# Optimization experiments

Hardware: AMD Instinct MI355X
Metric: run time of the kernel (lower is better)

## Reference

```python
import jax, jax.numpy as jnp
from jax import lax
import numpy as np

VOCAB = 100000
EMB = 256
HID = 512          # bidirectional total
H = HID // 2       # per-direction hidden
TAGS = 12
START_IDX = 10
STOP_IDX = 11
B, S = 32, 256
NEG = -10000.0


def setup_inputs() -> dict:
    key = jax.random.key(0)
    ks = jax.random.split(key, 14)
    sc = 0.1
    sentences = jax.random.randint(ks[0], (B, S), 0, VOCAB)
    emb = jax.random.normal(ks[1], (VOCAB, EMB), jnp.float32) * sc
    wih_f = jax.random.normal(ks[2], (4 * H, EMB), jnp.float32) * sc
    whh_f = jax.random.normal(ks[3], (4 * H, H), jnp.float32) * sc
    bih_f = jax.random.normal(ks[4], (4 * H,), jnp.float32) * sc
    bhh_f = jax.random.normal(ks[5], (4 * H,), jnp.float32) * sc
    wih_b = jax.random.normal(ks[6], (4 * H, EMB), jnp.float32) * sc
    whh_b = jax.random.normal(ks[7], (4 * H, H), jnp.float32) * sc
    bih_b = jax.random.normal(ks[8], (4 * H,), jnp.float32) * sc
    bhh_b = jax.random.normal(ks[9], (4 * H,), jnp.float32) * sc
    w_out = jax.random.normal(ks[10], (TAGS, HID), jnp.float32) * sc
    b_out = jax.random.normal(ks[11], (TAGS,), jnp.float32) * sc
    transitions = jax.random.normal(ks[12], (TAGS, TAGS), jnp.float32)
    transitions = transitions.at[START_IDX, :].set(NEG)   # never transition into START
    transitions = transitions.at[:, STOP_IDX].set(NEG)    # never transition out of STOP
    return dict(sentences=sentences, emb=emb, wih_f=wih_f, whh_f=whh_f,
                bih_f=bih_f, bhh_f=bhh_f, wih_b=wih_b, whh_b=whh_b,
                bih_b=bih_b, bhh_b=bhh_b, w_out=w_out, b_out=b_out,
                transitions=transitions)


def _lstm_dir(x, wih, whh, bih, bhh, reverse):
    # x: [B,S,E]; PyTorch gate order i,f,g,o
    xg = jnp.einsum('bse,ge->bsg', x, wih) + bih + bhh  # [B,S,4H]
    h0 = jnp.zeros((x.shape[0], whh.shape[1]), x.dtype)
    c0 = jnp.zeros_like(h0)

    def step(carry, g_t):
        h, c = carry
        g = g_t + h @ whh.T
        i, f, gg, o = jnp.split(g, 4, axis=-1)
        c = jax.nn.sigmoid(f) * c + jax.nn.sigmoid(i) * jnp.tanh(gg)
        h = jax.nn.sigmoid(o) * jnp.tanh(c)
        return (h, c), h

    _, hs = lax.scan(step, (h0, c0), jnp.swapaxes(xg, 0, 1), reverse=reverse)
    return jnp.swapaxes(hs, 0, 1)  # [B,S,H]


def _features(sentences, emb, wih_f, whh_f, bih_f, bhh_f,
              wih_b, whh_b, bih_b, bhh_b, w_out, b_out):
    x = emb[sentences]                                   # [B,S,E]
    hf = _lstm_dir(x, wih_f, whh_f, bih_f, bhh_f, False)
    hb = _lstm_dir(x, wih_b, whh_b, bih_b, bhh_b, True)
    h = jnp.concatenate([hf, hb], axis=-1)               # [B,S,HID]
    return jnp.einsum('bsh,th->bst', h, w_out) + b_out   # [B,S,TAGS]


def _viterbi(feats, transitions):
    # feats: [B,S,T]; returns (score [B], path [B,S] int32)
    T = feats.shape[-1]
    init = jnp.full((T,), NEG, feats.dtype).at[START_IDX].set(0.0)

    def step(fv, emit):
        scores = fv[None, :] + transitions               # [next_tag, prev_tag]
        bp = jnp.argmax(scores, axis=1).astype(jnp.int32)
        fv_new = jnp.max(scores, axis=1) + emit
        return fv_new, bp

    def per_seq(feat_seq):                               # [S,T]
        fv, bps = lax.scan(step, init, feat_seq)         # bps: [S,T]
        term = fv + transitions[STOP_IDX]
        best = jnp.argmax(term).astype(jnp.int32)
        score = term[best]

        def back(tag, bp_t):
            return bp_t[tag], tag

        _, path = lax.scan(back, best, bps, reverse=True)
        return score, path

    return jax.vmap(per_seq)(feats)


def reference(sentences, emb, wih_f, whh_f, bih_f, bhh_f,
              wih_b, whh_b, bih_b, bhh_b, w_out, b_out, transitions):
    feats = _features(sentences, emb, wih_f, whh_f, bih_f, bhh_f,
                      wih_b, whh_b, bih_b, bhh_b, w_out, b_out)
    score, path = _viterbi(feats, transitions)
    return score, path
```

## Files before the change

kernel.cpp:

```cpp
#include <hip/hip_runtime.h>
#include <math.h>

#define BATCH 32
#define SEQ 256
#define EMBD 256
#define HDIM 256
#define G4H 1024
#define TAGS 12
#define START_IDX 10
#define STOP_IDX 11
#define NEGV -10000.0f

#define KRES 48
#define KLDS_G 18
#define KSTR_G 34

#define WS_XG    0
#define WS_X     16777216
#define WS_WPACK 18874368
#define WS_HALL  19234816
#define WS_FEATS 23429120

__device__ __forceinline__ float bcast(float v, int l) {
    return __int_as_float(__builtin_amdgcn_readlane(__float_as_int(v), l));
}

__global__ void gather_x(const int* __restrict__ sent, const float* __restrict__ emb,
                         float* __restrict__ x) {
    int m = blockIdx.x;
    int lane = threadIdx.x;
    long long row = sent[m];
    float4 v = *(const float4*)(emb + row * EMBD + lane * 4);
    *(float4*)(x + (size_t)m * EMBD + lane * 4) = v;
}

__global__ void pack_whh(const float* __restrict__ whh_f, const float* __restrict__ whh_b,
                         float4* __restrict__ pack) {
    int idx = blockIdx.x * 256 + threadIdx.x;
    if (idx >= 2 * 2 * KSTR_G * 512) return;
    int g = idx & 511;
    int r = idx >> 9;
    int j = r % KSTR_G; r /= KSTR_G;
    int half = r & 1, dir = r >> 1;
    int R = (g >> 7) * 256 + half * 128 + (g & 127);
    const float* w = dir ? whh_b : whh_f;
    pack[idx] = *(const float4*)(w + (size_t)R * HDIM + KRES + 4 * KLDS_G + 4 * j);
}

__launch_bounds__(256)
__global__ void gemm_xg(const float* __restrict__ x,
                        const float* __restrict__ wih_f, const float* __restrict__ wih_b,
                        const float* __restrict__ bih_f, const float* __restrict__ bhh_f,
                        const float* __restrict__ bih_b, const float* __restrict__ bhh_b,
                        float* __restrict__ xg) {
    __shared__ __align__(16) float as[8][128];
    __shared__ __align__(16) float bs[8][128];
    int m0 = blockIdx.x * 128;
    int n0 = blockIdx.y * 128;
    int tid = threadIdx.x;
    int tx = tid & 15, ty = tid >> 4;
    int lr = tid >> 1;
    int lh = (tid & 1) * 4;

    const float* arow = x + (size_t)(m0 + lr) * EMBD;
    const float* brow;
    {
        int n = n0 + lr;
        const float* w = (n < G4H) ? wih_f : wih_b;
        brow = w + (size_t)(n & 1023) * EMBD;
    }

    float acc[8][8];
    #pragma unroll
    for (int i = 0; i < 8; i++)
        #pragma unroll
        for (int j = 0; j < 8; j++) acc[i][j] = 0.f;

    for (int k0 = 0; k0 < EMBD; k0 += 8) {
        float4 av = *(const float4*)(arow + k0 + lh);
        float4 bv = *(const float4*)(brow + k0 + lh);
        __syncthreads();
        as[lh + 0][lr] = av.x; as[lh + 1][lr] = av.y; as[lh + 2][lr] = av.z; as[lh + 3][lr] = av.w;
        bs[lh + 0][lr] = bv.x; bs[lh + 1][lr] = bv.y; bs[lh + 2][lr] = bv.z; bs[lh + 3][lr] = bv.w;
        __syncthreads();
        #pragma unroll
        for (int kk = 0; kk < 8; kk++) {
            float4 a0 = *(const float4*)&as[kk][ty * 8];
            float4 a1 = *(const float4*)&as[kk][ty * 8 + 4];
            float4 b0 = *(const float4*)&bs[kk][tx * 8];
            float4 b1 = *(const float4*)&bs[kk][tx * 8 + 4];
            float a[8] = {a0.x, a0.y, a0.z, a0.w, a1.x, a1.y, a1.z, a1.w};
            float b[8] = {b0.x, b0.y, b0.z, b0.w, b1.x, b1.y, b1.z, b1.w};
            #pragma unroll
            for (int i = 0; i < 8; i++)
                #pragma unroll
                for (int j = 0; j < 8; j++) acc[i][j] += a[i] * b[j];
        }
    }

    int n = n0 + tx * 8;
    int dir = n >> 10, g0 = n & 1023;
    const float* bih = dir ? bih_b : bih_f;
    const float* bhh = dir ? bhh_b : bhh_f;
    float bi[8], bh[8];
    #pragma unroll
    for (int j = 0; j < 8; j++) { bi[j] = bih[g0 + j]; bh[j] = bhh[g0 + j]; }
    float* ob = xg + (size_t)dir * 8192 * G4H;
    #pragma unroll
    for (int i = 0; i < 8; i++) {
        int m = m0 + ty * 8 + i;
        float v[8];
        #pragma unroll
        for (int j = 0; j < 8; j++) v[j] = (acc[i][j] + bi[j]) + bh[j];
        *(float4*)(ob + (size_t)m * G4H + g0)     = make_float4(v[0], v[1], v[2], v[3]);
        *(float4*)(ob + (size_t)m * G4H + g0 + 4) = make_float4(v[4], v[5], v[6], v[7]);
    }
}

__global__ void zero_sync(float* __restrict__ hx, int* __restrict__ flags) {
    int i = blockIdx.x * 256 + threadIdx.x;
    if (i < 64 * 512) hx[i] = 0.f;
    if (i < 128) flags[i] = 0;
}

#define DOT4(W, K)                                              \
    a0 += (W).x * bcast(hv[((K) + 0) >> 6], ((K) + 0) & 63);    \
    a1 += (W).y * bcast(hv[((K) + 1) >> 6], ((K) + 1) & 63);    \
    a2 += (W).z * bcast(hv[((K) + 2) >> 6], ((K) + 2) & 63);    \
    a3 += (W).w * bcast(hv[((K) + 3) >> 6], ((K) + 3) & 63);

__launch_bounds__(512)
__global__ void lstm_rec(const float* __restrict__ xg,
                         const float* __restrict__ whh_f, const float* __restrict__ whh_b,
                         const float4* __restrict__ wpack,
                         float* __restrict__ h_all,
                         float* __restrict__ hx, int* __restrict__ flags) {
    int blk = blockIdx.x;
    int half = blk & 1;
    int chain = blk >> 1;
    int dir = chain & 1, b = chain >> 1;
    int g = threadIdx.x;
    int lane = g & 63;
    int unit0 = half * 128;
    int R = (g >> 7) * 256 + unit0 + (g & 127);

    const float* whh = dir ? whh_b : whh_f;
    const float4* wp = wpack + (size_t)(dir * 2 + half) * KSTR_G * 512 + g;
    const float* xgb = xg + (size_t)dir * 8192 * G4H + (size_t)b * SEQ * G4H + R;
    float* hxc = hx + chain * 512;
    int* own_flag = flags + chain * 2 + half;
    int* par_flag = flags + chain * 2 + (1 - half);

    __shared__ __align__(16) float4 wlds[KLDS_G * 512];
    __shared__ float gates[512];

    #pragma unroll
    for (int j = 0; j < KLDS_G; j++)
        wlds[j * 512 + g] = *(const float4*)(whh + (size_t)R * HDIM + KRES + j * 4);
    float4 wr[KRES / 4];
    #pragma unroll
    for (int i = 0; i < KRES / 4; i++)
        wr[i] = *(const float4*)(whh + (size_t)R * HDIM + i * 4);

    float c = 0.f;
    __syncthreads();

    for (int t = 0; t < SEQ; t++) {
        int s = dir ? (SEQ - 1 - t) : t;

        float xval = xgb[(size_t)s * G4H];
        float4 sb[4];
        #pragma unroll
        for (int p = 0; p < 4; p++) sb[p] = wp[(size_t)p * 512];

        if (t > 0) {
            if (g == 0)
                while (__hip_atomic_load(par_flag, __ATOMIC_ACQUIRE,
                                         __HIP_MEMORY_SCOPE_AGENT) < t) {}
            __syncthreads();
        }

        int rp = (t + 1) & 1;
        float hv[4];
        #pragma unroll
        for (int j = 0; j < 4; j++)
            hv[j] = __hip_atomic_load(hxc + rp * 256 + j * 64 + lane,
                                      __ATOMIC_RELAXED, __HIP_MEMORY_SCOPE_AGENT);

        float a0 = xval, a1 = 0.f, a2 = 0.f, a3 = 0.f;

        #pragma unroll
        for (int i = 0; i < KRES / 4; i++) {
            float4 w = wr[i];
            DOT4(w, i * 4)
        }
        #pragma unroll
        for (int j = 0; j < KLDS_G; j++) {
            float4 w = wlds[j * 512 + g];
            DOT4(w, KRES + j * 4)
        }
        #pragma unroll
        for (int j = 0; j < KSTR_G; j++) {
            float4 w = sb[j & 3];
            if (j + 4 < KSTR_G) sb[j & 3] = wp[(size_t)(j + 4) * 512];
            DOT4(w, KRES + 4 * KLDS_G + j * 4)
        }

        gates[g] = (a0 + a1) + (a2 + a3);
        __syncthreads();
        if (g < 128) {
            float gi = gates[g], gf = gates[128 + g], gg = gates[256 + g], go = gates[384 + g];
            float si = 1.f / (1.f + expf(-gi));
            float sf = 1.f / (1.f + expf(-gf));
            float so = 1.f / (1.f + expf(-go));
            c = sf * c + si * tanhf(gg);
            float h = so * tanhf(c);
            int u = unit0 + g;
            h_all[((size_t)b * SEQ + s) * 512 + dir * HDIM + u] = h;
            __hip_atomic_store(hxc + (t & 1) * 256 + u, h,
                               __ATOMIC_RELAXED, __HIP_MEMORY_SCOPE_AGENT);
        }
        __syncthreads();
        if (g == 0)
            __hip_atomic_store(own_flag, t + 1,
                               __ATOMIC_RELEASE, __HIP_MEMORY_SCOPE_AGENT);
    }
}

__global__ void feats_kernel(const float* __restrict__ h_all, const float* __restrict__ w_out,
                             const float* __restrict__ b_out, float* __restrict__ feats) {
    int p = blockIdx.x;
    int lane = threadIdx.x;
    const float* h = h_all + (size_t)p * 512;
    for (int f = 0; f < TAGS; f++) {
        float s = 0.f;
        const float* w = w_out + f * 512;
        #pragma unroll
        for (int k = 0; k < 512; k += 64) s += h[k + lane] * w[k + lane];
        #pragma unroll
        for (int off = 32; off; off >>= 1) s += __shfl_down(s, off);
        if (lane == 0) feats[(size_t)p * TAGS + f] = s + b_out[f];
    }
}

__global__ void viterbi_kernel(const float* __restrict__ feats, const float* __restrict__ trans,
                               float* __restrict__ out) {
    int b = blockIdx.x;
    int t = threadIdx.x;
    __shared__ float fv[TAGS], fvn[TAGS], tr[TAGS * TAGS];
    __shared__ int bp[SEQ][TAGS];

    for (int i = t; i < TAGS * TAGS; i += 64) tr[i] = trans[i];
    if (t < TAGS) fv[t] = (t == START_IDX) ? 0.f : NEGV;
    __syncthreads();

    const float* fb = feats + (size_t)b * SEQ * TAGS;
    for (int s = 0; s < SEQ; s++) {
        if (t < TAGS) {
            float best = fv[0] + tr[t * TAGS + 0];
            int bi = 0;
            #pragma unroll
            for (int prev = 1; prev < TAGS; prev++) {
                float v = fv[prev] + tr[t * TAGS + prev];
                if (v > best) { best = v; bi = prev; }
            }
            bp[s][t] = bi;
            fvn[t] = best + fb[s * TAGS + t];
        }
        __syncthreads();
        if (t < TAGS) fv[t] = fvn[t];
        __syncthreads();
    }

    if (t == 0) {
        float best = fv[0] + tr[STOP_IDX * TAGS + 0];
        int bi = 0;
        #pragma unroll
        for (int p = 1; p < TAGS; p++) {
            float v = fv[p] + tr[STOP_IDX * TAGS + p];
            if (v > best) { best = v; bi = p; }
        }
        out[b] = best;
        float* path = out + BATCH + (size_t)b * SEQ;
        int tag = bi;
        path[SEQ - 1] = (float)tag;
        for (int s = SEQ - 1; s >= 1; s--) {
            tag = bp[s][tag];
            path[s - 1] = (float)tag;
        }
    }
}

extern "C" void kernel_launch(void* const* d_in, const int* in_sizes, int n_in,
                              void* d_out, int out_size, void* d_ws, size_t ws_size,
                              hipStream_t stream) {
    const int*   sent  = (const int*)d_in[0];
    const float* emb   = (const float*)d_in[1];
    const float* wih_f = (const float*)d_in[2];
    const float* whh_f = (const float*)d_in[3];
    const float* bih_f = (const float*)d_in[4];
    const float* bhh_f = (const float*)d_in[5];
    const float* wih_b = (const float*)d_in[6];
    const float* whh_b = (const float*)d_in[7];
    const float* bih_b = (const float*)d_in[8];
    const float* bhh_b = (const float*)d_in[9];
    const float* w_out = (const float*)d_in[10];
    const float* b_out = (const float*)d_in[11];
    const float* trans = (const float*)d_in[12];
    float* ws    = (float*)d_ws;
    float* xg    = ws + WS_XG;
    float* x     = ws + WS_X;
    float* wpack = ws + WS_WPACK;
    float* h_all = ws + WS_HALL;
    float* feats = ws + WS_FEATS;
    float* hx    = ws + WS_X;
    int*   flags = (int*)(ws + WS_X + 64 * 512);
    float* out   = (float*)d_out;

    gather_x<<<BATCH * SEQ, 64, 0, stream>>>(sent, emb, x);
    pack_whh<<<(2 * 2 * KSTR_G * 512 + 255) / 256, 256, 0, stream>>>(whh_f, whh_b, (float4*)wpack);
    gemm_xg<<<dim3(64, 16), 256, 0, stream>>>(x, wih_f, wih_b, bih_f, bhh_f, bih_b, bhh_b, xg);
    zero_sync<<<128, 256, 0, stream>>>(hx, flags);
    lstm_rec<<<128, 512, 0, stream>>>(xg, whh_f, whh_b, (const float4*)wpack, h_all, hx, flags);
    feats_kernel<<<BATCH * SEQ, 64, 0, stream>>>(h_all, w_out, b_out, feats);
    viterbi_kernel<<<BATCH, 64, 0, stream>>>(feats, trans, out);
}
```

Baseline: 1.593 ms.

## Compute own-half hidden contribution before waiting on partner block flag

Each block now keeps its own half of the hidden state in shared memory and does the dot product over those 128 units, streamed from the packed weights with an 8-deep ring, before spinning on the partner's flag. Only the partner's 128 units are read from global memory after the wait, using register- and LDS-resident weights. This moves work off the critical cross-block sync path so it overlaps with the wait, at the cost of repacking the weights and more registers for the larger prefetch ring.

New measurement: 1.552 ms. -2.6%, faster.

```diff
diff --git a/kernel.cpp b/kernel.cpp
--- a/kernel.cpp
+++ b/kernel.cpp
@@ -11,9 +11,12 @@
 #define STOP_IDX 11
 #define NEGV -10000.0f
 
-#define KRES 48
-#define KLDS_G 18
+#define KV 48
+#define KL_G 18
+#define PT_G 2
+#define OWN_G 32
 #define KSTR_G 34
+#define RING 8
 
 #define WS_XG    0
 #define WS_X     16777216
@@ -42,9 +45,11 @@
     int r = idx >> 9;
     int j = r % KSTR_G; r /= KSTR_G;
     int half = r & 1, dir = r >> 1;
-    int R = (g >> 7) * 256 + half * 128 + (g & 127);
+    int o0 = half * 128, p0 = 128 - o0;
+    int R = (g >> 7) * 256 + o0 + (g & 127);
+    int k = (j < PT_G) ? (p0 + KV + 4 * KL_G + 4 * j) : (o0 + 4 * (j - PT_G));
     const float* w = dir ? whh_b : whh_f;
-    pack[idx] = *(const float4*)(w + (size_t)R * HDIM + KRES + 4 * KLDS_G + 4 * j);
+    pack[idx] = *(const float4*)(w + (size_t)R * HDIM + k);
 }
 
 __launch_bounds__(256)
@@ -123,11 +128,11 @@
     if (i < 128) flags[i] = 0;
 }
 
-#define DOT4(W, K)                                              \
-    a0 += (W).x * bcast(hv[((K) + 0) >> 6], ((K) + 0) & 63);    \
-    a1 += (W).y * bcast(hv[((K) + 1) >> 6], ((K) + 1) & 63);    \
-    a2 += (W).z * bcast(hv[((K) + 2) >> 6], ((K) + 2) & 63);    \
-    a3 += (W).w * bcast(hv[((K) + 3) >> 6], ((K) + 3) & 63);
+#define DOT4(W, HV, KL)                                              \
+    a0 += (W).x * bcast(HV[((KL) + 0) >> 6], ((KL) + 0) & 63);       \
+    a1 += (W).y * bcast(HV[((KL) + 1) >> 6], ((KL) + 1) & 63);       \
+    a2 += (W).z * bcast(HV[((KL) + 2) >> 6], ((KL) + 2) & 63);       \
+    a3 += (W).w * bcast(HV[((KL) + 3) >> 6], ((KL) + 3) & 63);
 
 __launch_bounds__(512)
 __global__ void lstm_rec(const float* __restrict__ xg,
@@ -142,36 +147,54 @@
     int g = threadIdx.x;
     int lane = g & 63;
     int unit0 = half * 128;
+    int p0 = 128 - unit0;
     int R = (g >> 7) * 256 + unit0 + (g & 127);
 
     const float* whh = dir ? whh_b : whh_f;
+    const float* wrow = whh + (size_t)R * HDIM;
     const float4* wp = wpack + (size_t)(dir * 2 + half) * KSTR_G * 512 + g;
     const float* xgb = xg + (size_t)dir * 8192 * G4H + (size_t)b * SEQ * G4H + R;
     float* hxc = hx + chain * 512;
     int* own_flag = flags + chain * 2 + half;
     int* par_flag = flags + chain * 2 + (1 - half);
 
-    __shared__ __align__(16) float4 wlds[KLDS_G * 512];
+    __shared__ __align__(16) float4 wlds[KL_G * 512];
     __shared__ float gates[512];
-
-    #pragma unroll
-    for (int j = 0; j < KLDS_G; j++)
-        wlds[j * 512 + g] = *(const float4*)(whh + (size_t)R * HDIM + KRES + j * 4);
-    float4 wr[KRES / 4];
-    #pragma unroll
-    for (int i = 0; i < KRES / 4; i++)
-        wr[i] = *(const float4*)(whh + (size_t)R * HDIM + i * 4);
+    __shared__ float h_own[128];
+
+    #pragma unroll
+    for (int j = 0; j < KL_G; j++)
+        wlds[j * 512 + g] = *(const float4*)(wrow + p0 + KV + j * 4);
+    float4 wr[KV / 4];
+    #pragma unroll
+    for (int i = 0; i < KV / 4; i++)
+        wr[i] = *(const float4*)(wrow + p0 + i * 4);
 
     float c = 0.f;
+    if (g < 128) h_own[g] = 0.f;
     __syncthreads();
 
     for (int t = 0; t < SEQ; t++) {
         int s = dir ? (SEQ - 1 - t) : t;
 
         float xval = xgb[(size_t)s * G4H];
-        float4 sb[4];
-        #pragma unroll
-        for (int p = 0; p < 4; p++) sb[p] = wp[(size_t)p * 512];
+        float4 sbB[2];
+        sbB[0] = wp[0 * 512]; sbB[1] = wp[1 * 512];
+        float4 sb[RING];
+        #pragma unroll
+        for (int p = 0; p < RING; p++) sb[p] = wp[(size_t)(PT_G + p) * 512];
+
+        float hvo[2];
+        #pragma unroll
+        for (int j = 0; j < 2; j++) hvo[j] = h_own[j * 64 + lane];
+
+        float a0 = xval, a1 = 0.f, a2 = 0.f, a3 = 0.f;
+        #pragma unroll
+        for (int j = 0; j < OWN_G; j++) {
+            float4 w = sb[j & (RING - 1)];
+            if (j + RING < OWN_G) sb[j & (RING - 1)] = wp[(size_t)(PT_G + j + RING) * 512];
+            DOT4(w, hvo, j * 4)
+        }
 
         if (t > 0) {
             if (g == 0)
@@ -181,30 +204,24 @@
         }
 
         int rp = (t + 1) & 1;
-        float hv[4];
-        #pragma unroll
-        for (int j = 0; j < 4; j++)
-            hv[j] = __hip_atomic_load(hxc + rp * 256 + j * 64 + lane,
-                                      __ATOMIC_RELAXED, __HIP_MEMORY_SCOPE_AGENT);
-
-        float a0 = xval, a1 = 0.f, a2 = 0.f, a3 = 0.f;
-
-        #pragma unroll
-        for (int i = 0; i < KRES / 4; i++) {
+        float hvp[2];
+        #pragma unroll
+        for (int j = 0; j < 2; j++)
+            hvp[j] = __hip_atomic_load(hxc + rp * 256 + p0 + j * 64 + lane,
+                                       __ATOMIC_RELAXED, __HIP_MEMORY_SCOPE_AGENT);
+
+        #pragma unroll
+        for (int i = 0; i < KV / 4; i++) {
             float4 w = wr[i];
-            DOT4(w, i * 4)
-        }
-        #pragma unroll
-        for (int j = 0; j < KLDS_G; j++) {
+            DOT4(w, hvp, i * 4)
+        }
+        #pragma unroll
+        for (int j = 0; j < KL_G; j++) {
             float4 w = wlds[j * 512 + g];
-            DOT4(w, KRES + j * 4)
-        }
-        #pragma unroll
-        for (int j = 0; j < KSTR_G; j++) {
-            float4 w = sb[j & 3];
-            if (j + 4 < KSTR_G) sb[j & 3] = wp[(size_t)(j + 4) * 512];
-            DOT4(w, KRES + 4 * KLDS_G + j * 4)
-        }
+            DOT4(w, hvp, KV + j * 4)
+        }
+        DOT4(sbB[0], hvp, KV + 4 * KL_G)
+        DOT4(sbB[1], hvp, KV + 4 * KL_G + 4)
 
         gates[g] = (a0 + a1) + (a2 + a3);
         __syncthreads();
@@ -216,6 +233,7 @@
             c = sf * c + si * tanhf(gg);
             float h = so * tanhf(c);
             int u = unit0 + g;
+            h_own[g] = h;
             h_all[((size_t)b * SEQ + s) * 512 + dir * HDIM + u] = h;
             __hip_atomic_store(hxc + (t & 1) * 256 + u, h,
                                __ATOMIC_RELAXED, __HIP_MEMORY_SCOPE_AGENT);
```
